# Kernel optimization log

Hardware: AMD Instinct MI355X
Metric: run time of the kernel (lower is better)

Reference implementation:

```python
import jax, jax.numpy as jnp
import numpy as np

EPS = 1e-5
LAMB = 1.0
N_VARS = 40000
N_EDGES = 200000
N_CONF = 100000
FEAT = 128
DOM = 4
T_MAX = 3


def setup_inputs() -> dict:
    key = jax.random.key(0)
    ks = jax.random.split(key, 16)
    # initial node states: torch.rand then row-normalized (F.normalize dim=1)
    s = jax.random.uniform(ks[0], (N_VARS, FEAT), dtype=jnp.float32)
    state0 = s / jnp.maximum(jnp.linalg.norm(s, axis=1, keepdims=True), 1e-12)
    def lin(k, fan_in, shape):
        return jax.random.normal(k, shape, dtype=jnp.float32) / np.sqrt(fan_in)
    inp = {
        'state0': state0,
        'W1': lin(ks[1], 2 * FEAT, (2 * FEAT, FEAT)),
        'b1': jnp.zeros((FEAT,), jnp.float32),
        'W2': lin(ks[2], FEAT, (FEAT, FEAT)),
        'b2': jnp.zeros((FEAT,), jnp.float32),
        'ln_g': jnp.ones((FEAT,), jnp.float32),
        'ln_b': jnp.zeros((FEAT,), jnp.float32),
        'bn_g': jnp.ones((FEAT,), jnp.float32),
        'bn_b': jnp.zeros((FEAT,), jnp.float32),
        'Wd': lin(ks[3], FEAT, (FEAT, DOM)),
        'bd': jnp.zeros((DOM,), jnp.float32),
        # positive relation/confidence matrices so -log(...) is finite
        'relation': jax.random.uniform(ks[4], (DOM, DOM), jnp.float32, 0.1, 1.0),
        'confidence_mat': jax.random.uniform(ks[5], (DOM, DOM), jnp.float32, 0.1, 1.0),
        # positive degrees (divisor)
        'degrees': jax.random.uniform(ks[6], (N_VARS,), jnp.float32, 1.0, 33.0),
        'idx_left': jax.random.randint(ks[7], (N_EDGES,), 0, N_VARS, jnp.int32),
        'idx_right': jax.random.randint(ks[8], (N_EDGES,), 0, N_VARS, jnp.int32),
        'idx_left_pos': jax.random.randint(ks[9], (N_CONF,), 0, N_VARS, jnp.int32),
        'idx_right_pos': jax.random.randint(ks[10], (N_CONF,), 0, N_VARS, jnp.int32),
        'iterations': T_MAX,
    }
    return inp


def reference(state0, W1, b1, W2, b2, ln_g, ln_b, bn_g, bn_b, Wd, bd,
              relation, confidence_mat, degrees,
              idx_left, idx_right, idx_left_pos, idx_right_pos, iterations):
    N, F = state0.shape
    E = idx_left.shape[0]
    degs = degrees[:, None]

    def mlp(x):  # Linear-ReLU-Linear-ReLU-LayerNorm
        h = jax.nn.relu(x @ W1 + b1)
        h = jax.nn.relu(h @ W2 + b2)
        mu = jnp.mean(h, axis=-1, keepdims=True)
        var = jnp.var(h, axis=-1, keepdims=True)  # biased, like torch LayerNorm
        return ln_g * (h - mu) * jax.lax.rsqrt(var + EPS) + ln_b

    state = state0
    logits_list = []
    for _ in range(iterations):
        xl = state[idx_left]          # [E, F] gather
        xr = state[idx_right]
        # mpnn(in_right=xl, in_left=xr): in_lr = cat(xr, xl); in_rl = cat(xl, xr)
        msg = jnp.concatenate([jnp.concatenate([xr, xl], axis=1),
                               jnp.concatenate([xl, xr], axis=1)], axis=0)  # [2E, 2F]
        h = mlp(msg)
        agg = (jnp.zeros((N, F), state.dtype)
               .at[idx_left].add(h[:E])
               .at[idx_right].add(h[E:]))  # scatter-add messages
        rec = agg / degs
        # BatchNorm1d, training mode (batch stats over nodes)
        mu = jnp.mean(rec, axis=0)
        var = jnp.var(rec, axis=0)
        state = bn_g * (rec - mu) * jax.lax.rsqrt(var + EPS) + bn_b
        logits_list.append(state @ Wd + bd)

    phi = jax.nn.softmax(jnp.stack(logits_list, axis=1), axis=2)  # [N, T, D]
    T, D = phi.shape[1], phi.shape[2]
    all_phi = phi.reshape(N, T * D)

    def pair_loss(mat, il, ir, denom):
        pl = all_phi[il].reshape(-1, D)   # [E*T, D]
        pr = all_phi[ir].reshape(-1, D)
        s = jnp.sum((pl @ mat) * pr, axis=1)
        return jnp.sum(-jnp.log(s)) / denom

    n_conflicts = jnp.float32(E)
    n_confidence = jnp.float32(idx_left_pos.shape[0])
    loss = (pair_loss(relation, idx_left, idx_right, n_conflicts)
            + LAMB * pair_loss(confidence_mat, idx_left_pos, idx_right_pos, 10.0 * n_confidence))

    assignment = jnp.argmax(phi, axis=2).astype(jnp.int32)  # [N, T]
    valid = relation[assignment[idx_left], assignment[idx_right]]  # [E, T]
    edge_conflicts = 1.0 - valid
    n_conf = jnp.sum(edge_conflicts[:, -1])
    conflict_ratio = n_conf / n_conflicts
    return (loss, conflict_ratio, phi, edge_conflicts, assignment[:, -1], n_conf)
```

## Files before the change

### kernel.cpp

```cpp
#include <hip/hip_runtime.h>
#include <math.h>

#define N_VARS 40000
#define FEAT 128
#define N_EDGES 200000
#define N_MSG (2*N_EDGES)
#define N_CONFP 100000
#define T_ITERS 3
#define EPSF 1e-5f

#define NB_CONF 782
#define NB_LOSS 3517
#define NB_STAT 157
#define OUT_TOTAL 1120003
#define NCONF_SLOT 1120002

typedef short short8 __attribute__((ext_vector_type(8)));
typedef float floatx4 __attribute__((ext_vector_type(4)));
typedef unsigned short ushort4v __attribute__((ext_vector_type(4)));

__device__ __forceinline__ float scrub0(float x){
  unsigned u = __float_as_uint(x);
  return ((u & 0x7F800000u) == 0x7F800000u) ? 0.f : x;
}
__device__ __forceinline__ unsigned short f2bf_rne(float x){
  unsigned u = __float_as_uint(x);
  u += 0x7FFFu + ((u >> 16) & 1u);
  return (unsigned short)(u >> 16);
}
__device__ __forceinline__ float bf2f(unsigned short h){
  return __uint_as_float(((unsigned)h) << 16);
}

__global__ __launch_bounds__(256) void k_zero_agg(float4* __restrict__ p){
  p[blockIdx.x*256 + threadIdx.x] = make_float4(0.f,0.f,0.f,0.f);
}
__global__ __launch_bounds__(256) void k_zero_int(int* __restrict__ p, int n){
  int i = blockIdx.x*256 + threadIdx.x;
  if (i < n) p[i] = 0;
}

__global__ __launch_bounds__(256) void k_hist(const int* __restrict__ idxL,
    const int* __restrict__ idxR, int* __restrict__ cnt){
  int m = blockIdx.x*256 + threadIdx.x;
  if (m < N_MSG){
    int t = (m < N_EDGES) ? idxL[m] : idxR[m - N_EDGES];
    atomicAdd(&cnt[t], 1);
  }
}
__global__ __launch_bounds__(256) void k_scan1(const int* __restrict__ cnt,
    int* __restrict__ pos, int* __restrict__ blk_tot){
  const int tid = threadIdx.x;
  const int idx = blockIdx.x*256 + tid;
  int v = (idx < N_VARS) ? cnt[idx] : 0;
  __shared__ int sh[256];
  sh[tid] = v;
  __syncthreads();
#pragma unroll
  for (int o = 1; o < 256; o <<= 1){
    int add = (tid >= o) ? sh[tid - o] : 0;
    __syncthreads();
    sh[tid] += add;
    __syncthreads();
  }
  if (idx < N_VARS) pos[idx] = sh[tid] - v;
  if (tid == 255) blk_tot[blockIdx.x] = sh[255];
}
__global__ __launch_bounds__(256) void k_scan2(const int* __restrict__ blk_tot,
    int* __restrict__ blk_off){
  const int tid = threadIdx.x;
  int v = (tid < NB_STAT) ? blk_tot[tid] : 0;
  __shared__ int sh[256];
  sh[tid] = v;
  __syncthreads();
#pragma unroll
  for (int o = 1; o < 256; o <<= 1){
    int add = (tid >= o) ? sh[tid - o] : 0;
    __syncthreads();
    sh[tid] += add;
    __syncthreads();
  }
  if (tid < NB_STAT) blk_off[tid] = sh[tid] - v;
}
__global__ __launch_bounds__(256) void k_scan3(int* __restrict__ pos,
    const int* __restrict__ blk_off){
  const int idx = blockIdx.x*256 + threadIdx.x;
  if (idx < N_VARS) pos[idx] += blk_off[blockIdx.x];
}
__global__ __launch_bounds__(256) void k_fill(const int* __restrict__ idxL,
    const int* __restrict__ idxR, int* __restrict__ pos,
    int* __restrict__ morder, int* __restrict__ nodeof){
  int m = blockIdx.x*256 + threadIdx.x;
  if (m < N_MSG){
    int t = (m < N_EDGES) ? idxL[m] : idxR[m - N_EDGES];
    int slot = atomicAdd(&pos[t], 1);
    morder[slot] = m;
    nodeof[slot] = t;
  }
}

__global__ __launch_bounds__(256) void k_prep(const float* __restrict__ W2,
                                              unsigned short* __restrict__ W2pack){
  int gid = blockIdx.x*256 + threadIdx.x;
  int lane = gid & 63;
  int ks = (gid >> 6) & 3;
  int ntg = gid >> 8;
  int kbase = ks*32 + (lane >> 4)*8;
  int n = ntg*16 + (lane & 15);
#pragma unroll
  for (int j = 0; j < 8; ++j)
    W2pack[gid*8 + j] = f2bf_rne(W2[(kbase + j)*FEAT + n]);
}
__global__ __launch_bounds__(256) void k_prep_w1(const float* __restrict__ W1,
                                                 unsigned short* __restrict__ W1pack){
  int gid = blockIdx.x*256 + threadIdx.x;
  int lane = gid & 63;
  int ks = (gid >> 6) & 3;
  int ntg = gid >> 8;
  int kbase = ks*32 + (lane >> 4)*8;
  int n = ntg*16 + (lane & 15);
#pragma unroll
  for (int j = 0; j < 8; ++j){
    int k = kbase + j;
    float v = (n < 128) ? W1[k*FEAT + n] : W1[(128 + k)*FEAT + (n - 128)];
    W1pack[gid*8 + j] = f2bf_rne(v);
  }
}

#define X_STRIDE 136
__global__ __launch_bounds__(256) void k_pq(const float* __restrict__ xf,
                                            const unsigned short* __restrict__ xb,
                                            int src_f32,
                                            const unsigned short* __restrict__ W1pack,
                                            unsigned short* __restrict__ PQb,
                                            float* __restrict__ red){
  __shared__ __align__(16) unsigned short Xbf[32*X_STRIDE];
  const int tid = threadIdx.x;
  const int row0 = blockIdx.x * 32;
  if (blockIdx.x == 0) red[tid] = 0.f;
  if (src_f32){
    const int c4 = (tid & 31)*4, g8 = tid >> 5;
#pragma unroll
    for (int r = 0; r < 4; ++r){
      int row = g8*4 + r;
      const float4 v = *(const float4*)&xf[(row0 + row)*FEAT + c4];
      ushort4v u;
      u.x = f2bf_rne(v.x); u.y = f2bf_rne(v.y);
      u.z = f2bf_rne(v.z); u.w = f2bf_rne(v.w);
      *(ushort4v*)&Xbf[row*X_STRIDE + c4] = u;
    }
  } else {
    const int c8 = (tid & 15)*8, g16 = tid >> 4;
#pragma unroll
    for (int r = 0; r < 2; ++r){
      int row = r*16 + g16;
      *(short8*)&Xbf[row*X_STRIDE + c8] = *(const short8*)&xb[(row0 + row)*FEAT + c8];
    }
  }
  __syncthreads();
  const int w = tid >> 6, lane = tid & 63;
  const int quad = lane >> 4, mcol = lane & 15;
#pragma unroll
  for (int mt = 0; mt < 2; ++mt){
    floatx4 a0 = {0.f,0.f,0.f,0.f};
    floatx4 a1 = {0.f,0.f,0.f,0.f};
    floatx4 a2 = {0.f,0.f,0.f,0.f};
    floatx4 a3 = {0.f,0.f,0.f,0.f};
#pragma unroll
    for (int ks = 0; ks < 4; ++ks){
      short8 a = *(const short8*)&Xbf[(mt*16 + mcol)*X_STRIDE + ks*32 + quad*8];
      const unsigned short* bp = W1pack + ((w*16 + ks)*64 + lane)*8;
      short8 b0 = *(const short8*)(bp);
      short8 b1 = *(const short8*)(bp + 2048);
      short8 b2 = *(const short8*)(bp + 4096);
      short8 b3 = *(const short8*)(bp + 6144);
      a0 = __builtin_amdgcn_mfma_f32_16x16x32_bf16(a, b0, a0, 0, 0, 0);
      a1 = __builtin_amdgcn_mfma_f32_16x16x32_bf16(a, b1, a1, 0, 0, 0);
      a2 = __builtin_amdgcn_mfma_f32_16x16x32_bf16(a, b2, a2, 0, 0, 0);
      a3 = __builtin_amdgcn_mfma_f32_16x16x32_bf16(a, b3, a3, 0, 0, 0);
    }
#pragma unroll
    for (int nt = 0; nt < 4; ++nt){
      floatx4 acc = (nt == 0) ? a0 : (nt == 1) ? a1 : (nt == 2) ? a2 : a3;
      int n = w*64 + nt*16 + mcol;
#pragma unroll
      for (int reg = 0; reg < 4; ++reg)
        PQb[(row0 + mt*16 + quad*4 + reg)*(2*FEAT) + n] = f2bf_rne(acc[reg]);
    }
  }
}

#define U_STRIDE 136

__global__ __launch_bounds__(256) void k_msgagg(const unsigned short* __restrict__ PQb,
    const unsigned short* __restrict__ W2pack, const float* __restrict__ b1v,
    const float* __restrict__ b2v, const float* __restrict__ ln_g, const float* __restrict__ ln_b,
    const int* __restrict__ idxL, const int* __restrict__ idxR,
    const int* __restrict__ morder, const int* __restrict__ nodeof,
    float* __restrict__ rec){
  __shared__ __align__(16) unsigned short Ubf[64*U_STRIDE];
  __shared__ int sTa[64], sTb[64];
  __shared__ int sEdge[2];
  const int tid = threadIdx.x;
  const int s0 = blockIdx.x * 64;
  if (tid < 64){
    int m = morder[s0 + tid];
    int e = (m < N_EDGES) ? m : (m - N_EDGES);
    int l = idxL[e], r = idxR[e];
    sTa[tid] = (m < N_EDGES) ? l : r;
    sTb[tid] = (m < N_EDGES) ? r : l;
  } else if (tid == 64){
    sEdge[0] = (s0 == 0) ? -1 : nodeof[s0 - 1];
  } else if (tid == 65){
    sEdge[1] = (s0 + 64 >= N_MSG) ? -1 : nodeof[s0 + 64];
  }
  __syncthreads();
  {
    const int c8 = (tid & 15)*8, g16 = tid >> 4;
    const float4 b1a = *(const float4*)&b1v[c8];
    const float4 b1b = *(const float4*)&b1v[c8 + 4];
    short8 pb[4], qb[4];
#pragma unroll
    for (int r = 0; r < 4; ++r){
      int row = r*16 + g16;
      pb[r] = *(const short8*)&PQb[sTb[row]*(2*FEAT) + c8];
      qb[r] = *(const short8*)&PQb[sTa[row]*(2*FEAT) + FEAT + c8];
    }
#pragma unroll
    for (int r = 0; r < 4; ++r){
      int row = r*16 + g16;
      ushort4v u0, u1;
      u0.x = f2bf_rne(fmaxf(bf2f(pb[r][0]) + bf2f(qb[r][0]) + b1a.x, 0.f));
      u0.y = f2bf_rne(fmaxf(bf2f(pb[r][1]) + bf2f(qb[r][1]) + b1a.y, 0.f));
      u0.z = f2bf_rne(fmaxf(bf2f(pb[r][2]) + bf2f(qb[r][2]) + b1a.z, 0.f));
      u0.w = f2bf_rne(fmaxf(bf2f(pb[r][3]) + bf2f(qb[r][3]) + b1a.w, 0.f));
      u1.x = f2bf_rne(fmaxf(bf2f(pb[r][4]) + bf2f(qb[r][4]) + b1b.x, 0.f));
      u1.y = f2bf_rne(fmaxf(bf2f(pb[r][5]) + bf2f(qb[r][5]) + b1b.y, 0.f));
      u1.z = f2bf_rne(fmaxf(bf2f(pb[r][6]) + bf2f(qb[r][6]) + b1b.z, 0.f));
      u1.w = f2bf_rne(fmaxf(bf2f(pb[r][7]) + bf2f(qb[r][7]) + b1b.w, 0.f));
      *(ushort4v*)&Ubf[row*U_STRIDE + c8]     = u0;
      *(ushort4v*)&Ubf[row*U_STRIDE + c8 + 4] = u1;
    }
  }
  __syncthreads();
  const int w = tid >> 6, lane = tid & 63;
  const int quad = lane >> 4, mcol = lane & 15;
  const int rbase = w*16;
  floatx4 acc[8];
#pragma unroll
  for (int nt = 0; nt < 8; ++nt) acc[nt] = (floatx4){0.f,0.f,0.f,0.f};
#pragma unroll
  for (int ks = 0; ks < 4; ++ks){
    short8 a = *(const short8*)&Ubf[(rbase + mcol)*U_STRIDE + ks*32 + quad*8];
#pragma unroll
    for (int nt = 0; nt < 8; ++nt){
      short8 b = *(const short8*)(W2pack + ((nt*4 + ks)*64 + lane)*8);
      acc[nt] = __builtin_amdgcn_mfma_f32_16x16x32_bf16(a, b, acc[nt], 0, 0, 0);
    }
  }
  float z[8][4];
#pragma unroll
  for (int nt = 0; nt < 8; ++nt){
    float bb = b2v[nt*16 + mcol];
#pragma unroll
    for (int reg = 0; reg < 4; ++reg) z[nt][reg] = fmaxf(acc[nt][reg] + bb, 0.f);
  }
  float ps[4], pq[4];
#pragma unroll
  for (int reg = 0; reg < 4; ++reg){
    ps[reg] = 0.f; pq[reg] = 0.f;
#pragma unroll
    for (int nt = 0; nt < 8; ++nt){
      ps[reg] += z[nt][reg];
      pq[reg] += z[nt][reg]*z[nt][reg];
    }
  }
#pragma unroll
  for (int o = 1; o < 16; o <<= 1){
#pragma unroll
    for (int reg = 0; reg < 4; ++reg){
      ps[reg] += __shfl_xor(ps[reg], o);
      pq[reg] += __shfl_xor(pq[reg], o);
    }
  }
  float lgv[8], lbv[8];
#pragma unroll
  for (int nt = 0; nt < 8; ++nt){
    lgv[nt] = ln_g[nt*16 + mcol];
    lbv[nt] = ln_b[nt*16 + mcol];
  }
  unsigned short ob[4][8];
#pragma unroll
  for (int reg = 0; reg < 4; ++reg){
    float mu = ps[reg] * (1.f/FEAT);
    float var = fmaxf(pq[reg] * (1.f/FEAT) - mu*mu, 0.f);
    float rv = rsqrtf(var + EPSF);
#pragma unroll
    for (int nt = 0; nt < 8; ++nt)
      ob[reg][nt] = f2bf_rne(scrub0(lgv[nt]*(z[nt][reg] - mu)*rv + lbv[nt]));
  }
  __syncthreads();
#pragma unroll
  for (int reg = 0; reg < 4; ++reg){
    int row = rbase + quad*4 + reg;
#pragma unroll
    for (int nt = 0; nt < 8; ++nt)
      Ubf[row*U_STRIDE + nt*16 + mcol] = ob[reg][nt];
  }
  __syncthreads();
  if (tid < 128){
    const int col = tid;
    float accv = 0.f;
    int cur = sTa[0];
    bool part = (sEdge[0] == cur);
    for (int r = 0; r < 64; ++r){
      accv += bf2f(Ubf[r*U_STRIDE + col]);
      int nxt = (r < 63) ? sTa[r + 1] : -2;
      if (nxt != cur){
        bool tail = (r == 63) && (sEdge[1] == cur);
        float* dst = &rec[(size_t)cur*FEAT + col];
        if (part | tail) atomicAdd(dst, accv);
        else *dst = accv;
        accv = 0.f;
        cur = nxt;
        part = false;
      }
    }
  }
}

__global__ __launch_bounds__(256) void k_edge(const unsigned short* __restrict__ PQb,
    const unsigned short* __restrict__ W2pack, const float* __restrict__ b1v,
    const float* __restrict__ b2v, const float* __restrict__ ln_g, const float* __restrict__ ln_b,
    const int* __restrict__ idxL, const int* __restrict__ idxR,
    float* __restrict__ agg){
  __shared__ __align__(16) unsigned short Ubf[32*U_STRIDE];
  __shared__ float sS[64], sQ[64];
  __shared__ int sTa[32], sTb[32];
  const int tid = threadIdx.x;
  const int m0 = blockIdx.x * 32;
  if (tid < 32){
    int m = m0 + tid;
    int e = (m < N_EDGES) ? m : (m - N_EDGES);
    int l = idxL[e], r = idxR[e];
    sTa[tid] = (m < N_EDGES) ? l : r;
    sTb[tid] = (m < N_EDGES) ? r : l;
  }
  __syncthreads();
  {
    const int c8 = (tid & 15)*8, g16 = tid >> 4;
    const float4 b1a = *(const float4*)&b1v[c8];
    const float4 b1b = *(const float4*)&b1v[c8 + 4];
#pragma unroll
    for (int r = 0; r < 2; ++r){
      int row = r*16 + g16;
      short8 pb = *(const short8*)&PQb[sTb[row]*(2*FEAT) + c8];
      short8 qb = *(const short8*)&PQb[sTa[row]*(2*FEAT) + FEAT + c8];
      ushort4v u0, u1;
      u0.x = f2bf_rne(fmaxf(bf2f(pb[0]) + bf2f(qb[0]) + b1a.x, 0.f));
      u0.y = f2bf_rne(fmaxf(bf2f(pb[1]) + bf2f(qb[1]) + b1a.y, 0.f));
      u0.z = f2bf_rne(fmaxf(bf2f(pb[2]) + bf2f(qb[2]) + b1a.z, 0.f));
      u0.w = f2bf_rne(fmaxf(bf2f(pb[3]) + bf2f(qb[3]) + b1a.w, 0.f));
      u1.x = f2bf_rne(fmaxf(bf2f(pb[4]) + bf2f(qb[4]) + b1b.x, 0.f));
      u1.y = f2bf_rne(fmaxf(bf2f(pb[5]) + bf2f(qb[5]) + b1b.y, 0.f));
      u1.z = f2bf_rne(fmaxf(bf2f(pb[6]) + bf2f(qb[6]) + b1b.z, 0.f));
      u1.w = f2bf_rne(fmaxf(bf2f(pb[7]) + bf2f(qb[7]) + b1b.w, 0.f));
      *(ushort4v*)&Ubf[row*U_STRIDE + c8]     = u0;
      *(ushort4v*)&Ubf[row*U_STRIDE + c8 + 4] = u1;
    }
  }
  __syncthreads();
  const int w = tid >> 6, lane = tid & 63;
  const int mt = w & 1, nhalf = w >> 1;
  const int quad = lane >> 4, mcol = lane & 15;
  floatx4 acc0 = {0.f,0.f,0.f,0.f};
  floatx4 acc1 = {0.f,0.f,0.f,0.f};
  floatx4 acc2 = {0.f,0.f,0.f,0.f};
  floatx4 acc3 = {0.f,0.f,0.f,0.f};
#pragma unroll
  for (int ks = 0; ks < 4; ++ks){
    short8 a = *(const short8*)&Ubf[(mt*16 + mcol)*U_STRIDE + ks*32 + quad*8];
    const unsigned short* bp = W2pack + ((nhalf*4*256) + ks*64 + lane)*8;
    short8 bq0 = *(const short8*)(bp);
    short8 bq1 = *(const short8*)(bp + 2048);
    short8 bq2 = *(const short8*)(bp + 4096);
    short8 bq3 = *(const short8*)(bp + 6144);
    acc0 = __builtin_amdgcn_mfma_f32_16x16x32_bf16(a, bq0, acc0, 0, 0, 0);
    acc1 = __builtin_amdgcn_mfma_f32_16x16x32_bf16(a, bq1, acc1, 0, 0, 0);
    acc2 = __builtin_amdgcn_mfma_f32_16x16x32_bf16(a, bq2, acc2, 0, 0, 0);
    acc3 = __builtin_amdgcn_mfma_f32_16x16x32_bf16(a, bq3, acc3, 0, 0, 0);
  }
  float z[4][4];
#pragma unroll
  for (int nt = 0; nt < 4; ++nt){
    floatx4 a4 = (nt == 0) ? acc0 : (nt == 1) ? acc1 : (nt == 2) ? acc2 : acc3;
    float bb = b2v[nhalf*64 + nt*16 + mcol];
#pragma unroll
    for (int reg = 0; reg < 4; ++reg) z[nt][reg] = fmaxf(a4[reg] + bb, 0.f);
  }
  float ps[4], pq[4];
#pragma unroll
  for (int reg = 0; reg < 4; ++reg){
    ps[reg] = z[0][reg] + z[1][reg] + z[2][reg] + z[3][reg];
    pq[reg] = z[0][reg]*z[0][reg] + z[1][reg]*z[1][reg] + z[2][reg]*z[2][reg] + z[3][reg]*z[3][reg];
  }
#pragma unroll
  for (int o = 1; o < 16; o <<= 1){
#pragma unroll
    for (int reg = 0; reg < 4; ++reg){
      ps[reg] += __shfl_xor(ps[reg], o);
      pq[reg] += __shfl_xor(pq[reg], o);
    }
  }
  if (mcol == 0){
#pragma unroll
    for (int reg = 0; reg < 4; ++reg){
      int row = mt*16 + quad*4 + reg;
      sS[nhalf*32 + row] = ps[reg];
      sQ[nhalf*32 + row] = pq[reg];
    }
  }
  __syncthreads();
  int colv[4]; float lgv[4], lbv[4];
#pragma unroll
  for (int nt = 0; nt < 4; ++nt){
    colv[nt] = nhalf*64 + nt*16 + mcol;
    lgv[nt] = ln_g[colv[nt]];
    lbv[nt] = ln_b[colv[nt]];
  }
#pragma unroll
  for (int reg = 0; reg < 4; ++reg){
    int row = mt*16 + quad*4 + reg;
    float s = sS[row] + sS[32 + row];
    float q = sQ[row] + sQ[32 + row];
    float mu = s * (1.f/FEAT);
    float var = fmaxf(q * (1.f/FEAT) - mu*mu, 0.f);
    float rv = rsqrtf(var + EPSF);
    int a = sTa[row];
#pragma unroll
    for (int nt = 0; nt < 4; ++nt){
      float o = scrub0(lgv[nt]*(z[nt][reg] - mu)*rv + lbv[nt]);
      atomicAdd(&agg[a*FEAT + colv[nt]], o);
    }
  }
}

__global__ __launch_bounds__(256) void k_stats(const float* __restrict__ src,
    const float* __restrict__ degrees, float* __restrict__ red){
  const int tid = threadIdx.x;
  const int j = tid & 127, half_sel = tid >> 7;
  const int n0 = blockIdx.x * 256;
  float s1 = 0.f, s2 = 0.f;
  for (int i = half_sel; i < 256; i += 2){
    int n = n0 + i;
    if (n < N_VARS){
      float v = src[n*FEAT + j] / degrees[n];
      s1 += v;
      s2 += v*v;
    }
  }
  __shared__ float sh1[256], sh2[256];
  sh1[tid] = s1; sh2[tid] = s2;
  __syncthreads();
  if (half_sel == 0){
    atomicAdd(&red[j],       sh1[tid] + sh1[tid+128]);
    atomicAdd(&red[128 + j], sh2[tid] + sh2[tid+128]);
  }
}

__global__ __launch_bounds__(256) void k_bn(const float* __restrict__ src,
    const float* __restrict__ degrees, int divide, const float* __restrict__ red,
    const float* __restrict__ bn_g, const float* __restrict__ bn_b,
    const float* __restrict__ Wd, const float* __restrict__ bd,
    unsigned short* __restrict__ state_bf, int* __restrict__ asg,
    float* __restrict__ out_phi, float* __restrict__ out_asg, int t){
  const int w = threadIdx.x >> 6, l = threadIdx.x & 63;
  const int n = blockIdx.x*4 + w;
  const float invN = 1.f / (float)N_VARS;
  float mu0 = red[l]*invN,     mu1 = red[l+64]*invN;
  float v0  = fmaxf(red[128+l]*invN    - mu0*mu0, 0.f);
  float v1  = fmaxf(red[128+l+64]*invN - mu1*mu1, 0.f);
  float rv0 = rsqrtf(v0 + EPSF);
  float rv1 = rsqrtf(v1 + EPSF);
  float dinv = divide ? (1.f / degrees[n]) : 1.f;
  float r0 = src[n*FEAT + l]    * dinv;
  float r1 = src[n*FEAT + l+64] * dinv;
  float s0 = scrub0(bn_g[l]   *(r0 - mu0)*rv0 + bn_b[l]);
  float s1 = scrub0(bn_g[l+64]*(r1 - mu1)*rv1 + bn_b[l+64]);
  state_bf[n*FEAT + l]    = f2bf_rne(s0);
  state_bf[n*FEAT + l+64] = f2bf_rne(s1);
  float p[4];
#pragma unroll
  for (int d = 0; d < 4; ++d)
    p[d] = s0*Wd[l*4 + d] + s1*Wd[(l+64)*4 + d];
#pragma unroll
  for (int o = 32; o > 0; o >>= 1){
#pragma unroll
    for (int d = 0; d < 4; ++d) p[d] += __shfl_xor(p[d], o);
  }
  if (l == 0){
    float lg[4];
#pragma unroll
    for (int d = 0; d < 4; ++d) lg[d] = scrub0(p[d] + bd[d]);
    float mx = fmaxf(fmaxf(lg[0],lg[1]), fmaxf(lg[2],lg[3]));
    float ex[4]; float ssum = 0.f;
#pragma unroll
    for (int d = 0; d < 4; ++d){ ex[d] = expf(lg[d] - mx); ssum += ex[d]; }
    float inv = 1.f / ssum;
    int am = 0; float bv = -1.f;
#pragma unroll
    for (int d = 0; d < 4; ++d){
      float pv = scrub0(ex[d]*inv);
      out_phi[n*12 + t*4 + d] = pv;
      if (pv > bv){ bv = pv; am = d; }
    }
    asg[n*3 + t] = am;
    if (t == 2) out_asg[n] = (float)am;
  }
}

__global__ __launch_bounds__(256) void k_lossconf(const float* __restrict__ phi,
    const int* __restrict__ iL, const int* __restrict__ iR,
    const int* __restrict__ iLp, const int* __restrict__ iRp,
    const float* __restrict__ rel, const float* __restrict__ conf,
    const int* __restrict__ asg, float* __restrict__ out_ec,
    float* __restrict__ part_l1, float* __restrict__ part_l2,
    float* __restrict__ part_conf){
  if (blockIdx.x < NB_LOSS){
    const int m = blockIdx.x*256 + threadIdx.x;
    float p1 = 0.f, p2 = 0.f;
    if (m < N_EDGES*3){
      int e = m/3, tt = m - e*3;
      const float* pl = phi + iL[e]*12 + tt*4;
      const float* pr = phi + iR[e]*12 + tt*4;
      float s = 0.f;
#pragma unroll
      for (int j = 0; j < 4; ++j){
        float tj = 0.f;
#pragma unroll
        for (int i = 0; i < 4; ++i) tj += pl[i]*rel[i*4+j];
        s += tj*pr[j];
      }
      s = scrub0(s); s = fmaxf(s, 1e-35f);
      p1 = -logf(s);
    } else {
      int m2 = m - N_EDGES*3;
      if (m2 < N_CONFP*3){
        int e = m2/3, tt = m2 - e*3;
        const float* pl = phi + iLp[e]*12 + tt*4;
        const float* pr = phi + iRp[e]*12 + tt*4;
        float s = 0.f;
#pragma unroll
        for (int j = 0; j < 4; ++j){
          float tj = 0.f;
#pragma unroll
          for (int i = 0; i < 4; ++i) tj += pl[i]*conf[i*4+j];
          s += tj*pr[j];
        }
        s = scrub0(s); s = fmaxf(s, 1e-35f);
        p2 = -logf(s);
      }
    }
    __shared__ float sh1[256], sh2[256];
    sh1[threadIdx.x] = p1; sh2[threadIdx.x] = p2;
    __syncthreads();
    for (int k = 128; k > 0; k >>= 1){
      if (threadIdx.x < k){
        sh1[threadIdx.x] += sh1[threadIdx.x + k];
        sh2[threadIdx.x] += sh2[threadIdx.x + k];
      }
      __syncthreads();
    }
    if (threadIdx.x == 0){
      part_l1[blockIdx.x] = sh1[0];
      part_l2[blockIdx.x] = sh2[0];
    }
  } else {
    const int bid = blockIdx.x - NB_LOSS;
    const int e = bid*256 + threadIdx.x;
    float c2 = 0.f;
    if (e < N_EDGES){
      int l = iL[e], r = iR[e];
#pragma unroll
      for (int tt = 0; tt < 3; ++tt){
        int ai = asg[l*3+tt] & 3, bi = asg[r*3+tt] & 3;
        float c = scrub0(1.f - rel[ai*4 + bi]);
        out_ec[e*3 + tt] = c;
        if (tt == 2) c2 = c;
      }
    }
    __shared__ float sh[256];
    sh[threadIdx.x] = c2;
    __syncthreads();
    for (int k = 128; k > 0; k >>= 1){
      if (threadIdx.x < k) sh[threadIdx.x] += sh[threadIdx.x + k];
      __syncthreads();
    }
    if (threadIdx.x == 0) part_conf[bid] = sh[0];
  }
}

__global__ __launch_bounds__(256) void k_fin(const float* __restrict__ part_conf,
    const float* __restrict__ part_l1, const float* __restrict__ part_l2,
    float* __restrict__ out){
  const int tid = threadIdx.x;
  float a = 0.f, ca = 0.f, b = 0.f, cb = 0.f, c = 0.f;
  for (int i = tid; i < NB_LOSS; i += 256){
    float y = part_l1[i] - ca; float t = a + y; ca = (t - a) - y; a = t;
    float y2 = part_l2[i] - cb; float t2 = b + y2; cb = (t2 - b) - y2; b = t2;
  }
  for (int i = tid; i < NB_CONF; i += 256) c += part_conf[i];
  __shared__ float sh1[256], sh2[256], sh3[256];
  sh1[tid] = a; sh2[tid] = b; sh3[tid] = c;
  __syncthreads();
  for (int k = 128; k > 0; k >>= 1){
    if (tid < k){
      sh1[tid] += sh1[tid + k];
      sh2[tid] += sh2[tid + k];
      sh3[tid] += sh3[tid + k];
    }
    __syncthreads();
  }
  if (tid == 0){
    out[0] = sh1[0]/(float)N_EDGES + sh2[0]/(10.f*(float)N_CONFP);
    float nc = sh3[0];
    out[NCONF_SLOT] = nc;
    out[1] = nc / (float)N_EDGES;
  }
}

extern "C" void kernel_launch(void* const* d_in, const int* in_sizes, int n_in,
                              void* d_out, int out_size, void* d_ws, size_t ws_size,
                              hipStream_t stream){
  const float* state0  = (const float*)d_in[0];
  const float* W1      = (const float*)d_in[1];
  const float* b1v     = (const float*)d_in[2];
  const float* W2      = (const float*)d_in[3];
  const float* b2v     = (const float*)d_in[4];
  const float* ln_g    = (const float*)d_in[5];
  const float* ln_b    = (const float*)d_in[6];
  const float* bn_g    = (const float*)d_in[7];
  const float* bn_b    = (const float*)d_in[8];
  const float* Wd      = (const float*)d_in[9];
  const float* bd      = (const float*)d_in[10];
  const float* rel     = (const float*)d_in[11];
  const float* confm   = (const float*)d_in[12];
  const float* degrees = (const float*)d_in[13];
  const int* idxL = (const int*)d_in[14];
  const int* idxR = (const int*)d_in[15];
  const int* iLp  = (const int*)d_in[16];
  const int* iRp  = (const int*)d_in[17];

  char* ws = (char*)d_ws;
  unsigned short* state_bf = (unsigned short*)(ws);
  unsigned short* PQb  = (unsigned short*)(ws + 10240000);
  float*  recagg    = (float*)(ws + 30720000);
  int*    asg       = (int*)  (ws + 51200000);
  float*  red       = (float*)(ws + 51840768);
  float*  part_l1   = (float*)(ws + 51841792);
  float*  part_l2   = (float*)(ws + 51855860);
  float*  part_conf = (float*)(ws + 51869928);
  unsigned short* W2pack = (unsigned short*)(ws + 51873056);
  unsigned short* W1pack = (unsigned short*)(ws + 51905824);
  int*    pos       = (int*)(ws + 51971360);
  int*    cnt       = (int*)(ws + 52131360);
  int*    morder    = (int*)(ws + 52291360);
  int*    blk_tot   = (int*)(ws + 53891360);
  int*    blk_off   = (int*)(ws + 53892384);
  int*    nodeof    = (int*)(ws + 53893408);
  const int use_csr = (ws_size >= (size_t)55493408) ? 1 : 0;

  float* out     = (float*)d_out;
  float* out_phi = out + 2;
  float* out_ec  = out + 480002;
  float* out_asg = out + 1080002;

  k_prep<<<8, 256, 0, stream>>>(W2, W2pack);
  k_prep_w1<<<16, 256, 0, stream>>>(W1, W1pack);

  if (use_csr){
    k_zero_int<<<NB_STAT, 256, 0, stream>>>(cnt, N_VARS);
    k_hist<<<(N_MSG + 255)/256, 256, 0, stream>>>(idxL, idxR, cnt);
    k_scan1<<<NB_STAT, 256, 0, stream>>>(cnt, pos, blk_tot);
    k_scan2<<<1, 256, 0, stream>>>(blk_tot, blk_off);
    k_scan3<<<NB_STAT, 256, 0, stream>>>(pos, blk_off);
    k_fill<<<(N_MSG + 255)/256, 256, 0, stream>>>(idxL, idxR, pos, morder, nodeof);
  }

  for (int t = 0; t < T_ITERS; ++t){
    k_pq<<<N_VARS/32, 256, 0, stream>>>(state0, state_bf, (t == 0) ? 1 : 0, W1pack, PQb, red);
    k_zero_agg<<<5000, 256, 0, stream>>>((float4*)recagg);
    if (use_csr){
      k_msgagg<<<N_MSG/64, 256, 0, stream>>>(PQb, W2pack, b1v, b2v, ln_g, ln_b,
                                             idxL, idxR, morder, nodeof, recagg);
    } else {
      k_edge<<<N_MSG/32, 256, 0, stream>>>(PQb, W2pack, b1v, b2v, ln_g, ln_b, idxL, idxR, recagg);
    }
    k_stats<<<NB_STAT, 256, 0, stream>>>(recagg, degrees, red);
    k_bn<<<N_VARS/4, 256, 0, stream>>>(recagg, degrees, 1, red, bn_g, bn_b, Wd, bd,
                                       state_bf, asg, out_phi, out_asg, t);
  }
  k_lossconf<<<NB_LOSS + NB_CONF, 256, 0, stream>>>(out_phi, idxL, idxR, iLp, iRp, rel, confm,
                                                    asg, out_ec, part_l1, part_l2, part_conf);
  k_fin<<<1, 256, 0, stream>>>(part_conf, part_l1, part_l2, out);
}
```

Before: 629.3 us.

## Fuse bias, zeroing and degree division into GEMM and segmented-reduce kernels

Zeroing of the aggregation buffer moves into the projection kernel, removing a separate launch. The first-layer bias is folded into the Q half of the projection output, and the second-layer bias is used as the accumulator's initial value. Division by node degree moves into the segmented reduction, so the stats and BN kernels skip it. The segmented reduce now uses a transposed LDS layout and all 256 threads over two row halves, and conversions use packed v_cvt_pk_bf16_f32. Folding bias before bf16 rounding slightly changes numerics, and the split-half reduce adds more atomics at half boundaries.

New measurement: 563.1 us. 1.12x faster.

```diff
diff --git a/kernel.cpp b/kernel.cpp
--- a/kernel.cpp
+++ b/kernel.cpp
@@ -31,10 +31,12 @@
 __device__ __forceinline__ float bf2f(unsigned short h){
   return __uint_as_float(((unsigned)h) << 16);
 }
-
-__global__ __launch_bounds__(256) void k_zero_agg(float4* __restrict__ p){
-  p[blockIdx.x*256 + threadIdx.x] = make_float4(0.f,0.f,0.f,0.f);
-}
+__device__ __forceinline__ unsigned cvtpk(float lo, float hi){
+  unsigned r;
+  asm("v_cvt_pk_bf16_f32 %0, %1, %2" : "=v"(r) : "v"(lo), "v"(hi));
+  return r;
+}
+
 __global__ __launch_bounds__(256) void k_zero_int(int* __restrict__ p, int n){
   int i = blockIdx.x*256 + threadIdx.x;
   if (i < n) p[i] = 0;
@@ -132,22 +134,30 @@
                                             const unsigned short* __restrict__ xb,
                                             int src_f32,
                                             const unsigned short* __restrict__ W1pack,
+                                            const float* __restrict__ b1v,
                                             unsigned short* __restrict__ PQb,
-                                            float* __restrict__ red){
+                                            float* __restrict__ red,
+                                            float4* __restrict__ recz){
   __shared__ __align__(16) unsigned short Xbf[32*X_STRIDE];
   const int tid = threadIdx.x;
   const int row0 = blockIdx.x * 32;
   if (blockIdx.x == 0) red[tid] = 0.f;
+  {
+    const int zid = blockIdx.x*256 + tid;
+#pragma unroll
+    for (int i = 0; i < 4; ++i)
+      recz[zid + i*320000] = make_float4(0.f,0.f,0.f,0.f);
+  }
   if (src_f32){
     const int c4 = (tid & 31)*4, g8 = tid >> 5;
 #pragma unroll
     for (int r = 0; r < 4; ++r){
       int row = g8*4 + r;
       const float4 v = *(const float4*)&xf[(row0 + row)*FEAT + c4];
-      ushort4v u;
-      u.x = f2bf_rne(v.x); u.y = f2bf_rne(v.y);
-      u.z = f2bf_rne(v.z); u.w = f2bf_rne(v.w);
-      *(ushort4v*)&Xbf[row*X_STRIDE + c4] = u;
+      uint2 uu;
+      uu.x = cvtpk(v.x, v.y);
+      uu.y = cvtpk(v.z, v.w);
+      *(uint2*)&Xbf[row*X_STRIDE + c4] = uu;
     }
   } else {
     const int c8 = (tid & 15)*8, g16 = tid >> 4;
@@ -160,12 +170,17 @@
   __syncthreads();
   const int w = tid >> 6, lane = tid & 63;
   const int quad = lane >> 4, mcol = lane & 15;
+  float bi0 = 0.f, bi1 = 0.f, bi2 = 0.f, bi3 = 0.f;
+  if (w >= 2){
+    int nb = (w - 2)*64 + mcol;
+    bi0 = b1v[nb]; bi1 = b1v[nb + 16]; bi2 = b1v[nb + 32]; bi3 = b1v[nb + 48];
+  }
 #pragma unroll
   for (int mt = 0; mt < 2; ++mt){
-    floatx4 a0 = {0.f,0.f,0.f,0.f};
-    floatx4 a1 = {0.f,0.f,0.f,0.f};
-    floatx4 a2 = {0.f,0.f,0.f,0.f};
-    floatx4 a3 = {0.f,0.f,0.f,0.f};
+    floatx4 a0 = {bi0,bi0,bi0,bi0};
+    floatx4 a1 = {bi1,bi1,bi1,bi1};
+    floatx4 a2 = {bi2,bi2,bi2,bi2};
+    floatx4 a3 = {bi3,bi3,bi3,bi3};
 #pragma unroll
     for (int ks = 0; ks < 4; ++ks){
       short8 a = *(const short8*)&Xbf[(mt*16 + mcol)*X_STRIDE + ks*32 + quad*8];
@@ -180,26 +195,31 @@
       a3 = __builtin_amdgcn_mfma_f32_16x16x32_bf16(a, b3, a3, 0, 0, 0);
     }
 #pragma unroll
-    for (int nt = 0; nt < 4; ++nt){
-      floatx4 acc = (nt == 0) ? a0 : (nt == 1) ? a1 : (nt == 2) ? a2 : a3;
-      int n = w*64 + nt*16 + mcol;
-#pragma unroll
-      for (int reg = 0; reg < 4; ++reg)
-        PQb[(row0 + mt*16 + quad*4 + reg)*(2*FEAT) + n] = f2bf_rne(acc[reg]);
+    for (int reg = 0; reg < 4; ++reg){
+      unsigned u01 = cvtpk(a0[reg], a1[reg]);
+      unsigned u23 = cvtpk(a2[reg], a3[reg]);
+      size_t base = (size_t)(row0 + mt*16 + quad*4 + reg)*(2*FEAT) + w*64 + mcol;
+      PQb[base]      = (unsigned short)u01;
+      PQb[base + 16] = (unsigned short)(u01 >> 16);
+      PQb[base + 32] = (unsigned short)u23;
+      PQb[base + 48] = (unsigned short)(u23 >> 16);
     }
   }
 }
 
 #define U_STRIDE 136
+#define ZT_STRIDE 68
 
 __global__ __launch_bounds__(256) void k_msgagg(const unsigned short* __restrict__ PQb,
-    const unsigned short* __restrict__ W2pack, const float* __restrict__ b1v,
+    const unsigned short* __restrict__ W2pack,
     const float* __restrict__ b2v, const float* __restrict__ ln_g, const float* __restrict__ ln_b,
     const int* __restrict__ idxL, const int* __restrict__ idxR,
     const int* __restrict__ morder, const int* __restrict__ nodeof,
+    const float* __restrict__ degrees,
     float* __restrict__ rec){
   __shared__ __align__(16) unsigned short Ubf[64*U_STRIDE];
   __shared__ int sTa[64], sTb[64];
+  __shared__ float sDinv[64];
   __shared__ int sEdge[2];
   const int tid = threadIdx.x;
   const int s0 = blockIdx.x * 64;
@@ -207,8 +227,10 @@
     int m = morder[s0 + tid];
     int e = (m < N_EDGES) ? m : (m - N_EDGES);
     int l = idxL[e], r = idxR[e];
-    sTa[tid] = (m < N_EDGES) ? l : r;
+    int ta = (m < N_EDGES) ? l : r;
+    sTa[tid] = ta;
     sTb[tid] = (m < N_EDGES) ? r : l;
+    sDinv[tid] = 1.f / degrees[ta];
   } else if (tid == 64){
     sEdge[0] = (s0 == 0) ? -1 : nodeof[s0 - 1];
   } else if (tid == 65){
@@ -217,8 +239,6 @@
   __syncthreads();
   {
     const int c8 = (tid & 15)*8, g16 = tid >> 4;
-    const float4 b1a = *(const float4*)&b1v[c8];
-    const float4 b1b = *(const float4*)&b1v[c8 + 4];
     short8 pb[4], qb[4];
 #pragma unroll
     for (int r = 0; r < 4; ++r){
@@ -229,17 +249,16 @@
 #pragma unroll
     for (int r = 0; r < 4; ++r){
       int row = r*16 + g16;
-      ushort4v u0, u1;
-      u0.x = f2bf_rne(fmaxf(bf2f(pb[r][0]) + bf2f(qb[r][0]) + b1a.x, 0.f));
-      u0.y = f2bf_rne(fmaxf(bf2f(pb[r][1]) + bf2f(qb[r][1]) + b1a.y, 0.f));
-      u0.z = f2bf_rne(fmaxf(bf2f(pb[r][2]) + bf2f(qb[r][2]) + b1a.z, 0.f));
-      u0.w = f2bf_rne(fmaxf(bf2f(pb[r][3]) + bf2f(qb[r][3]) + b1a.w, 0.f));
-      u1.x = f2bf_rne(fmaxf(bf2f(pb[r][4]) + bf2f(qb[r][4]) + b1b.x, 0.f));
-      u1.y = f2bf_rne(fmaxf(bf2f(pb[r][5]) + bf2f(qb[r][5]) + b1b.y, 0.f));
-      u1.z = f2bf_rne(fmaxf(bf2f(pb[r][6]) + bf2f(qb[r][6]) + b1b.z, 0.f));
-      u1.w = f2bf_rne(fmaxf(bf2f(pb[r][7]) + bf2f(qb[r][7]) + b1b.w, 0.f));
-      *(ushort4v*)&Ubf[row*U_STRIDE + c8]     = u0;
-      *(ushort4v*)&Ubf[row*U_STRIDE + c8 + 4] = u1;
+      float f[8];
+#pragma unroll
+      for (int j = 0; j < 8; ++j)
+        f[j] = fmaxf(bf2f((unsigned short)pb[r][j]) + bf2f((unsigned short)qb[r][j]), 0.f);
+      uint4 uu;
+      uu.x = cvtpk(f[0], f[1]);
+      uu.y = cvtpk(f[2], f[3]);
+      uu.z = cvtpk(f[4], f[5]);
+      uu.w = cvtpk(f[6], f[7]);
+      *(uint4*)&Ubf[row*U_STRIDE + c8] = uu;
     }
   }
   __syncthreads();
@@ -248,7 +267,10 @@
   const int rbase = w*16;
   floatx4 acc[8];
 #pragma unroll
-  for (int nt = 0; nt < 8; ++nt) acc[nt] = (floatx4){0.f,0.f,0.f,0.f};
+  for (int nt = 0; nt < 8; ++nt){
+    float b = b2v[nt*16 + mcol];
+    acc[nt] = (floatx4){b, b, b, b};
+  }
 #pragma unroll
   for (int ks = 0; ks < 4; ++ks){
     short8 a = *(const short8*)&Ubf[(rbase + mcol)*U_STRIDE + ks*32 + quad*8];
@@ -261,9 +283,8 @@
   float z[8][4];
 #pragma unroll
   for (int nt = 0; nt < 8; ++nt){
-    float bb = b2v[nt*16 + mcol];
-#pragma unroll
-    for (int reg = 0; reg < 4; ++reg) z[nt][reg] = fmaxf(acc[nt][reg] + bb, 0.f);
+#pragma unroll
+    for (int reg = 0; reg < 4; ++reg) z[nt][reg] = fmaxf(acc[nt][reg], 0.f);
   }
   float ps[4], pq[4];
 #pragma unroll
@@ -289,38 +310,53 @@
     lgv[nt] = ln_g[nt*16 + mcol];
     lbv[nt] = ln_b[nt*16 + mcol];
   }
-  unsigned short ob[4][8];
+  unsigned obp[4][4];
 #pragma unroll
   for (int reg = 0; reg < 4; ++reg){
     float mu = ps[reg] * (1.f/FEAT);
     float var = fmaxf(pq[reg] * (1.f/FEAT) - mu*mu, 0.f);
     float rv = rsqrtf(var + EPSF);
 #pragma unroll
-    for (int nt = 0; nt < 8; ++nt)
-      ob[reg][nt] = f2bf_rne(scrub0(lgv[nt]*(z[nt][reg] - mu)*rv + lbv[nt]));
+    for (int np = 0; np < 4; ++np){
+      float o0 = scrub0(lgv[2*np  ]*(z[2*np  ][reg] - mu)*rv + lbv[2*np  ]);
+      float o1 = scrub0(lgv[2*np+1]*(z[2*np+1][reg] - mu)*rv + lbv[2*np+1]);
+      obp[reg][np] = cvtpk(o0, o1);
+    }
   }
   __syncthreads();
 #pragma unroll
   for (int reg = 0; reg < 4; ++reg){
     int row = rbase + quad*4 + reg;
 #pragma unroll
-    for (int nt = 0; nt < 8; ++nt)
-      Ubf[row*U_STRIDE + nt*16 + mcol] = ob[reg][nt];
-  }
-  __syncthreads();
-  if (tid < 128){
-    const int col = tid;
+    for (int np = 0; np < 4; ++np){
+      unsigned u = obp[reg][np];
+      Ubf[(2*np*16 + mcol)*ZT_STRIDE + row]       = (unsigned short)u;
+      Ubf[((2*np+1)*16 + mcol)*ZT_STRIDE + row]   = (unsigned short)(u >> 16);
+    }
+  }
+  __syncthreads();
+  {
+    const int col = tid & 127, h = tid >> 7;
+    const int rbeg = h*32;
+    ushort4v rv4[8];
+#pragma unroll
+    for (int k = 0; k < 8; ++k)
+      rv4[k] = *(const ushort4v*)&Ubf[col*ZT_STRIDE + rbeg + k*4];
     float accv = 0.f;
-    int cur = sTa[0];
-    bool part = (sEdge[0] == cur);
-    for (int r = 0; r < 64; ++r){
-      accv += bf2f(Ubf[r*U_STRIDE + col]);
+    int cur = sTa[rbeg];
+    bool part = (rbeg == 0) ? (sEdge[0] == cur) : (sTa[rbeg-1] == cur);
+#pragma unroll
+    for (int i = 0; i < 32; ++i){
+      accv += bf2f((unsigned short)rv4[i >> 2][i & 3]);
+      const int r = rbeg + i;
       int nxt = (r < 63) ? sTa[r + 1] : -2;
-      if (nxt != cur){
-        bool tail = (r == 63) && (sEdge[1] == cur);
+      const bool lastr = (i == 31);
+      if (lastr | (nxt != cur)){
+        bool tail = lastr && ((r == 63) ? (sEdge[1] == cur) : (nxt == cur));
+        float v = accv * sDinv[r];
         float* dst = &rec[(size_t)cur*FEAT + col];
-        if (part | tail) atomicAdd(dst, accv);
-        else *dst = accv;
+        if (part | tail) atomicAdd(dst, v);
+        else *dst = v;
         accv = 0.f;
         cur = nxt;
         part = false;
@@ -330,7 +366,7 @@
 }
 
 __global__ __launch_bounds__(256) void k_edge(const unsigned short* __restrict__ PQb,
-    const unsigned short* __restrict__ W2pack, const float* __restrict__ b1v,
+    const unsigned short* __restrict__ W2pack,
     const float* __restrict__ b2v, const float* __restrict__ ln_g, const float* __restrict__ ln_b,
     const int* __restrict__ idxL, const int* __restrict__ idxR,
     float* __restrict__ agg){
@@ -349,34 +385,35 @@
   __syncthreads();
   {
     const int c8 = (tid & 15)*8, g16 = tid >> 4;
-    const float4 b1a = *(const float4*)&b1v[c8];
-    const float4 b1b = *(const float4*)&b1v[c8 + 4];
 #pragma unroll
     for (int r = 0; r < 2; ++r){
       int row = r*16 + g16;
       short8 pb = *(const short8*)&PQb[sTb[row]*(2*FEAT) + c8];
       short8 qb = *(const short8*)&PQb[sTa[row]*(2*FEAT) + FEAT + c8];
-      ushort4v u0, u1;
-      u0.x = f2bf_rne(fmaxf(bf2f(pb[0]) + bf2f(qb[0]) + b1a.x, 0.f));
-      u0.y = f2bf_rne(fmaxf(bf2f(pb[1]) + bf2f(qb[1]) + b1a.y, 0.f));
-      u0.z = f2bf_rne(fmaxf(bf2f(pb[2]) + bf2f(qb[2]) + b1a.z, 0.f));
-      u0.w = f2bf_rne(fmaxf(bf2f(pb[3]) + bf2f(qb[3]) + b1a.w, 0.f));
-      u1.x = f2bf_rne(fmaxf(bf2f(pb[4]) + bf2f(qb[4]) + b1b.x, 0.f));
-      u1.y = f2bf_rne(fmaxf(bf2f(pb[5]) + bf2f(qb[5]) + b1b.y, 0.f));
-      u1.z = f2bf_rne(fmaxf(bf2f(pb[6]) + bf2f(qb[6]) + b1b.z, 0.f));
-      u1.w = f2bf_rne(fmaxf(bf2f(pb[7]) + bf2f(qb[7]) + b1b.w, 0.f));
-      *(ushort4v*)&Ubf[row*U_STRIDE + c8]     = u0;
-      *(ushort4v*)&Ubf[row*U_STRIDE + c8 + 4] = u1;
+      float f[8];
+#pragma unroll
+      for (int j = 0; j < 8; ++j)
+        f[j] = fmaxf(bf2f((unsigned short)pb[j]) + bf2f((unsigned short)qb[j]), 0.f);
+      uint4 uu;
+      uu.x = cvtpk(f[0], f[1]);
+      uu.y = cvtpk(f[2], f[3]);
+      uu.z = cvtpk(f[4], f[5]);
+      uu.w = cvtpk(f[6], f[7]);
+      *(uint4*)&Ubf[row*U_STRIDE + c8] = uu;
     }
   }
   __syncthreads();
   const int w = tid >> 6, lane = tid & 63;
   const int mt = w & 1, nhalf = w >> 1;
   const int quad = lane >> 4, mcol = lane & 15;
-  floatx4 acc0 = {0.f,0.f,0.f,0.f};
-  floatx4 acc1 = {0.f,0.f,0.f,0.f};
-  floatx4 acc2 = {0.f,0.f,0.f,0.f};
-  floatx4 acc3 = {0.f,0.f,0.f,0.f};
+  float bb0 = b2v[nhalf*64 + 0*16 + mcol];
+  float bb1 = b2v[nhalf*64 + 1*16 + mcol];
+  float bb2 = b2v[nhalf*64 + 2*16 + mcol];
+  float bb3 = b2v[nhalf*64 + 3*16 + mcol];
+  floatx4 acc0 = {bb0,bb0,bb0,bb0};
+  floatx4 acc1 = {bb1,bb1,bb1,bb1};
+  floatx4 acc2 = {bb2,bb2,bb2,bb2};
+  floatx4 acc3 = {bb3,bb3,bb3,bb3};
 #pragma unroll
   for (int ks = 0; ks < 4; ++ks){
     short8 a = *(const short8*)&Ubf[(mt*16 + mcol)*U_STRIDE + ks*32 + quad*8];
@@ -394,9 +431,8 @@
 #pragma unroll
   for (int nt = 0; nt < 4; ++nt){
     floatx4 a4 = (nt == 0) ? acc0 : (nt == 1) ? acc1 : (nt == 2) ? acc2 : acc3;
-    float bb = b2v[nhalf*64 + nt*16 + mcol];
-#pragma unroll
-    for (int reg = 0; reg < 4; ++reg) z[nt][reg] = fmaxf(a4[reg] + bb, 0.f);
+#pragma unroll
+    for (int reg = 0; reg < 4; ++reg) z[nt][reg] = fmaxf(a4[reg], 0.f);
   }
   float ps[4], pq[4];
 #pragma unroll
@@ -446,7 +482,7 @@
 }
 
 __global__ __launch_bounds__(256) void k_stats(const float* __restrict__ src,
-    const float* __restrict__ degrees, float* __restrict__ red){
+    const float* __restrict__ degrees, int divide, float* __restrict__ red){
   const int tid = threadIdx.x;
   const int j = tid & 127, half_sel = tid >> 7;
   const int n0 = blockIdx.x * 256;
@@ -454,7 +490,8 @@
   for (int i = half_sel; i < 256; i += 2){
     int n = n0 + i;
     if (n < N_VARS){
-      float v = src[n*FEAT + j] / degrees[n];
+      float v = src[n*FEAT + j];
+      if (divide) v /= degrees[n];
       s1 += v;
       s2 += v*v;
     }
@@ -688,17 +725,20 @@
   }
 
   for (int t = 0; t < T_ITERS; ++t){
-    k_pq<<<N_VARS/32, 256, 0, stream>>>(state0, state_bf, (t == 0) ? 1 : 0, W1pack, PQb, red);
-    k_zero_agg<<<5000, 256, 0, stream>>>((float4*)recagg);
+    k_pq<<<N_VARS/32, 256, 0, stream>>>(state0, state_bf, (t == 0) ? 1 : 0, W1pack, b1v,
+                                        PQb, red, (float4*)recagg);
     if (use_csr){
-      k_msgagg<<<N_MSG/64, 256, 0, stream>>>(PQb, W2pack, b1v, b2v, ln_g, ln_b,
-                                             idxL, idxR, morder, nodeof, recagg);
+      k_msgagg<<<N_MSG/64, 256, 0, stream>>>(PQb, W2pack, b2v, ln_g, ln_b,
+                                             idxL, idxR, morder, nodeof, degrees, recagg);
+      k_stats<<<NB_STAT, 256, 0, stream>>>(recagg, degrees, 0, red);
+      k_bn<<<N_VARS/4, 256, 0, stream>>>(recagg, degrees, 0, red, bn_g, bn_b, Wd, bd,
+                                         state_bf, asg, out_phi, out_asg, t);
     } else {
-      k_edge<<<N_MSG/32, 256, 0, stream>>>(PQb, W2pack, b1v, b2v, ln_g, ln_b, idxL, idxR, recagg);
-    }
-    k_stats<<<NB_STAT, 256, 0, stream>>>(recagg, degrees, red);
-    k_bn<<<N_VARS/4, 256, 0, stream>>>(recagg, degrees, 1, red, bn_g, bn_b, Wd, bd,
-                                       state_bf, asg, out_phi, out_asg, t);
+      k_edge<<<N_MSG/32, 256, 0, stream>>>(PQb, W2pack, b2v, ln_g, ln_b, idxL, idxR, recagg);
+      k_stats<<<NB_STAT, 256, 0, stream>>>(recagg, degrees, 1, red);
+      k_bn<<<N_VARS/4, 256, 0, stream>>>(recagg, degrees, 1, red, bn_g, bn_b, Wd, bd,
+                                         state_bf, asg, out_phi, out_asg, t);
+    }
   }
   k_lossconf<<<NB_LOSS + NB_CONF, 256, 0, stream>>>(out_phi, idxL, idxR, iLp, iRp, rel, confm,
                                                     asg, out_ec, part_l1, part_l2, part_conf);
```
